# Optimization experiments

Measured on AMD Instinct MI355X. Metric: run time of the kernel, lower is better.

Reference implementation:

```python
import jax, jax.numpy as jnp
import numpy as np

C = 64          # channels
K = 7           # 19 - 6*num with num=2 (conv_first, avg_pool, snake kernel size)
GN_GROUPS = C // 4


def conv2d(x, w, b=None, pad=(0, 0), groups=1):
    out = jax.lax.conv_general_dilated(
        x, w, window_strides=(1, 1),
        padding=((pad[0], pad[0]), (pad[1], pad[1])),
        dimension_numbers=('NCHW', 'OIHW', 'NCHW'),
        feature_group_count=groups)
    if b is not None:
        out = out + b[None, :, None, None]
    return out


def avg_pool(x, k, pad):
    # torch AvgPool2d default count_include_pad=True -> always divide by k*k
    s = jax.lax.reduce_window(x, 0.0, jax.lax.add, (1, 1, k, k), (1, 1, 1, 1),
                              ((0, 0), (0, 0), (pad, pad), (pad, pad)))
    return s / float(k * k)


def bn_eval(x, g, b, m, v, eps):
    inv = g / jnp.sqrt(v + eps)
    return x * inv[None, :, None, None] + (b - m * inv)[None, :, None, None]


def group_norm(x, g, b, groups, eps=1e-5):
    B, Ch, H, W = x.shape
    xr = x.reshape(B, groups, Ch // groups, H, W)
    mu = xr.mean(axis=(2, 3, 4), keepdims=True)
    var = xr.var(axis=(2, 3, 4), keepdims=True)
    xr = (xr - mu) / jnp.sqrt(var + eps)
    return xr.reshape(B, Ch, H, W) * g[None, :, None, None] + b[None, :, None, None]


def cum_offset(off):
    # Faithful to DSCNet DSC: center point pinned to 0, offsets accumulate outward
    # via `for index in range(1, center)`. The two endpoints keep their RAW,
    # DETACHED offsets (original code's off-by-one quirk on the detached clone).
    k = off.shape[1]
    c = k // 2
    new = [None] * k
    new[c] = jnp.zeros_like(off[:, c])
    for i in range(1, c):
        new[c + i] = new[c + i - 1] + off[:, c + i]
        new[c - i] = new[c - i + 1] + off[:, c - i]
    new[0] = jax.lax.stop_gradient(off[:, 0])
    new[k - 1] = jax.lax.stop_gradient(off[:, k - 1])
    return jnp.stack(new, axis=1)


def bilinear(feat, y, x):
    # feat [B,C,R,Cc]; y,x [B,K,R,Cc] -> samples [B,C,K,R,Cc]
    B, Ch, R, Cc = feat.shape
    y0 = jnp.floor(y)
    x0 = jnp.floor(x)
    y0i = jnp.clip(y0.astype(jnp.int32), 0, R - 1)
    y1i = jnp.clip(y0.astype(jnp.int32) + 1, 0, R - 1)
    x0i = jnp.clip(x0.astype(jnp.int32), 0, Cc - 1)
    x1i = jnp.clip(x0.astype(jnp.int32) + 1, 0, Cc - 1)
    gather = jax.vmap(lambda f, yi, xi: f[:, yi, xi])  # [C,R,Cc],[K,R,Cc]->[C,K,R,Cc]
    va0 = gather(feat, y0i, x0i)
    vc0 = gather(feat, y0i, x1i)
    va1 = gather(feat, y1i, x0i)
    vc1 = gather(feat, y1i, x1i)
    # interpolation weights use coords clamped to [0, max+1] (faithful to original)
    y0f = jnp.clip(y0, 0.0, float(R))
    y1f = jnp.clip(y0 + 1.0, 0.0, float(R))
    x0f = jnp.clip(x0, 0.0, float(Cc))
    x1f = jnp.clip(x0 + 1.0, 0.0, float(Cc))
    wa0 = ((y1f - y) * (x1f - x))[:, None]
    wc0 = ((y1f - y) * (x - x0f))[:, None]
    wa1 = ((y - y0f) * (x1f - x))[:, None]
    wc1 = ((y - y0f) * (x - x0f))[:, None]
    return va0 * wa0 + vc0 * wc0 + va1 * wa1 + vc1 * wc1


def dsconv(x, off_w, off_b, bn_g, bn_b, bn_m, bn_v, dsc_w, dsc_b, gn_g, gn_b, morph):
    # Dynamic Snake Conv (extend_scope=1, if_offset=True)
    B, Ch, R, Cc = x.shape
    off = jnp.tanh(bn_eval(conv2d(x, off_w, off_b, (1, 1)), bn_g, bn_b, bn_m, bn_v, 1e-5))
    y_off, x_off = off[:, :K], off[:, K:]
    spread = (jnp.arange(K, dtype=x.dtype) - K // 2)[None, :, None, None]
    rows = jnp.arange(R, dtype=x.dtype)[None, None, :, None]
    cols = jnp.arange(Cc, dtype=x.dtype)[None, None, None, :]
    if morph == 0:  # kernel spreads along x, snake swings in y
        y = rows + cum_offset(y_off)
        xc = cols + spread
    else:           # kernel spreads along y, snake swings in x
        y = rows + spread
        xc = cols + cum_offset(x_off)
    y = jnp.broadcast_to(y, (B, K, R, Cc))
    xc = jnp.broadcast_to(xc, (B, K, R, Cc))
    samp = bilinear(x, y, xc)  # [B,C,K,R,Cc]
    # strided (K,1)/(1,K) conv over the deformed map == contraction over (in, k)
    out = jnp.einsum('oik,bikrc->borc', dsc_w, samp) + dsc_b[None, :, None, None]
    out = group_norm(out, gn_g, gn_b, GN_GROUPS)
    return jax.nn.relu(out)


def setup_inputs() -> dict:
    key = jax.random.key(0)
    kit = iter(jax.random.split(key, 64))

    def rn(shape):
        if len(shape) == 1:
            return jax.random.normal(next(kit), shape, jnp.float32) * 0.05
        fan_in = int(np.prod(shape[1:]))
        return jax.random.normal(next(kit), shape, jnp.float32) / np.sqrt(fan_in)

    B, H, W = 2, 192, 192
    d = {}
    d['x'] = jax.random.normal(next(kit), (B, C, H, W), jnp.float32)
    d['w_first'] = rn((C, C, K, K))
    d['hc1_w'] = rn((C, 1, 1, 9)); d['hc1_b'] = rn((C,))
    d['hc2_w'] = rn((C, 1, 1, 7)); d['hc2_b'] = rn((C,))
    d['hc3_w'] = rn((C, 1, 1, 5)); d['hc3_b'] = rn((C,))
    d['vc1_w'] = rn((C, 1, 9, 1)); d['vc1_b'] = rn((C,))
    d['vc2_w'] = rn((C, 1, 7, 1)); d['vc2_b'] = rn((C,))
    d['vc3_w'] = rn((C, 1, 5, 1)); d['vc3_b'] = rn((C,))
    for p in ('h', 'v'):
        d[p + '_off_w'] = rn((2 * K, C, 3, 3)); d[p + '_off_b'] = rn((2 * K,))
        d[p + '_bn_g'] = 1.0 + rn((2 * K,)); d[p + '_bn_b'] = rn((2 * K,))
        d[p + '_bn_m'] = rn((2 * K,))
        d[p + '_bn_v'] = jax.random.uniform(next(kit), (2 * K,), jnp.float32) + 0.5
        d[p + '_dsc_w'] = rn((C, C, K)); d[p + '_dsc_b'] = rn((C,))
        d[p + '_gn_g'] = 1.0 + rn((C,)); d[p + '_gn_b'] = rn((C,))
    d['last_w'] = rn((C, C, 1, 1))
    d['last_g'] = 1.0 + rn((C,)); d['last_b'] = rn((C,))
    d['last_m'] = rn((C,))
    d['last_v'] = jax.random.uniform(next(kit), (C,), jnp.float32) + 0.5
    return d


def reference(x, w_first, hc1_w, hc1_b, hc2_w, hc2_b, hc3_w, hc3_b,
              vc1_w, vc1_b, vc2_w, vc2_b, vc3_w, vc3_b,
              h_off_w, h_off_b, h_bn_g, h_bn_b, h_bn_m, h_bn_v,
              h_dsc_w, h_dsc_b, h_gn_g, h_gn_b,
              v_off_w, v_off_b, v_bn_g, v_bn_b, v_bn_m, v_bn_v,
              v_dsc_w, v_dsc_b, v_gn_g, v_gn_b,
              last_w, last_g, last_b, last_m, last_v):
    x1 = avg_pool(conv2d(x, w_first, None, (K // 2, K // 2)), K, K // 2)
    h = conv2d(x1, hc1_w, hc1_b, (0, 4), groups=C)
    h = conv2d(h, hc2_w, hc2_b, (0, 3), groups=C)
    h = conv2d(h, hc3_w, hc3_b, (0, 2), groups=C)
    h = dsconv(h, h_off_w, h_off_b, h_bn_g, h_bn_b, h_bn_m, h_bn_v,
               h_dsc_w, h_dsc_b, h_gn_g, h_gn_b, morph=0)
    v = conv2d(x1, vc1_w, vc1_b, (4, 0), groups=C)
    v = conv2d(v, vc2_w, vc2_b, (3, 0), groups=C)
    v = conv2d(v, vc3_w, vc3_b, (2, 0), groups=C)
    v = dsconv(v, v_off_w, v_off_b, v_bn_g, v_bn_b, v_bn_m, v_bn_v,
               v_dsc_w, v_dsc_b, v_gn_g, v_gn_b, morph=1)
    out = h + v + x1
    out = conv2d(out, last_w, None, (0, 0))          # 1x1, bias=False (norm present)
    out = bn_eval(out, last_g, last_b, last_m, last_v, 1e-3)
    return out * jax.nn.sigmoid(out)                  # SiLU
```

## Files before the change

### kernel.cpp

```cpp
#include <hip/hip_runtime.h>
#include <hip/hip_bf16.h>
#include <hip/hip_fp16.h>
#include <math.h>

#define Bq 2
#define Cq 64
#define Hq 192
#define Wq 192
#define HWq (Hq*Wq)
#define Nq ((size_t)Bq*Cq*HWq)

typedef __attribute__((ext_vector_type(8))) _Float16 f16x8;
typedef __attribute__((ext_vector_type(4))) float f32x4;

__device__ inline unsigned short h2us(__half h) {
  union { __half h; unsigned short u; } v; v.h = h; return v.u;
}

__global__ __launch_bounds__(256) void prep_all_kernel(
    const float* hc1_w, const float* hc1_b, const float* hc2_w, const float* hc2_b,
    const float* hc3_w, const float* hc3_b,
    const float* vc1_w, const float* vc1_b, const float* vc2_w, const float* vc2_b,
    const float* vc3_w, const float* vc3_b,
    const float* h_off_w, const float* h_off_b, const float* h_bn_g, const float* h_bn_b,
    const float* h_bn_m, const float* h_bn_v,
    const float* v_off_w, const float* v_off_b, const float* v_bn_g, const float* v_bn_b,
    const float* v_bn_m, const float* v_bn_v,
    const float* last_w, const float* last_g, const float* last_b, const float* last_m,
    const float* last_v,
    const float* __restrict__ w_first,
    const float* __restrict__ h_dsc_w, const float* __restrict__ v_dsc_w,
    float* wEffH, float* bEffH, float* wEffV, float* bEffV,
    float* wOffH, float* bOffH, float* wOffV, float* bOffV,
    float* lwT, float* lbO, float* wB,
    unsigned short* __restrict__ wtpH, unsigned short* __restrict__ wtpV,
    unsigned short* __restrict__ wpack)
{
  int bid = blockIdx.x;
  int t = threadIdx.x;
  if (bid == 0) {
    if (t < 128) {
      int ch = t & 63;
      bool ish = t < 64;
      const float* w1p = (ish ? hc1_w : vc1_w) + ch*9;
      const float* w2p = (ish ? hc2_w : vc2_w) + ch*7;
      const float* w3p = (ish ? hc3_w : vc3_w) + ch*5;
      float w1r[9], w2r[7], w3r[5];
#pragma unroll
      for (int j = 0; j < 9; j++) w1r[j] = w1p[j];
#pragma unroll
      for (int k = 0; k < 7; k++) w2r[k] = w2p[k];
#pragma unroll
      for (int m = 0; m < 5; m++) w3r[m] = w3p[m];
      float t15[15];
#pragma unroll
      for (int s = 0; s < 15; s++) {
        float a = 0.f;
#pragma unroll
        for (int j = 0; j < 9; j++) { int k2 = s - j; if (k2 >= 0 && k2 < 7) a += w1r[j]*w2r[k2]; }
        t15[s] = a;
      }
      float* we = (ish ? wEffH : wEffV) + ch*19;
#pragma unroll
      for (int s = 0; s < 19; s++) {
        float a = 0.f;
#pragma unroll
        for (int j = 0; j < 15; j++) { int k3 = s - j; if (k3 >= 0 && k3 < 5) a += t15[j]*w3r[k3]; }
        we[s] = a;
      }
      float S2 = 0.f, S3 = 0.f;
#pragma unroll
      for (int j = 0; j < 7; j++) S2 += w2r[j];
#pragma unroll
      for (int j = 0; j < 5; j++) S3 += w3r[j];
      float b1 = (ish ? hc1_b : vc1_b)[ch];
      float b2 = (ish ? hc2_b : vc2_b)[ch];
      float b3 = (ish ? hc3_b : vc3_b)[ch];
      (ish ? bEffH : bEffV)[ch] = b1*S2*S3 + b2*S3 + b3;
    }
    for (int idx = t; idx < 9*64*7; idx += 256) {
      int tap = idx / 448; int rem = idx % 448; int i = rem / 7; int m = rem % 7;
      float invh = h_bn_g[m] / sqrtf(h_bn_v[m] + 1e-5f);
      wOffH[(tap*64 + i)*8 + m] = h_off_w[(m*64 + i)*9 + tap] * invh;
      float invv = v_bn_g[7+m] / sqrtf(v_bn_v[7+m] + 1e-5f);
      wOffV[(tap*64 + i)*8 + m] = v_off_w[((7+m)*64 + i)*9 + tap] * invv;
    }
    if (t < 7) {
      float invh = h_bn_g[t] / sqrtf(h_bn_v[t] + 1e-5f);
      bOffH[t] = h_off_b[t]*invh + h_bn_b[t] - h_bn_m[t]*invh;
      float invv = v_bn_g[7+t] / sqrtf(v_bn_v[7+t] + 1e-5f);
      bOffV[t] = v_off_b[7+t]*invv + v_bn_b[7+t] - v_bn_m[7+t]*invv;
    }
    for (int idx = t; idx < 4096; idx += 256) {
      int o = idx % 64; int i = idx / 64;
      float inv = last_g[o] / sqrtf(last_v[o] + 1e-3f);
      lwT[i*64 + o] = last_w[o*64 + i] * inv;
    }
    if (t < 64) {
      float inv = last_g[t] / sqrtf(last_v[t] + 1e-3f);
      lbO[t] = last_b[t] - last_m[t]*inv;
    }
  } else if (bid <= 9) {
    int tid = (bid - 1)*256 + t;
    if (tid >= 2*64*18) return;
    int cls = tid % 18;
    int ch  = (tid / 18) % 64;
    int br  = tid / (18*64);
    int c = (cls < 9) ? cls : cls + 174;
    const float* w1p = (br==0 ? hc1_w : vc1_w) + ch*9;
    const float* w2p = (br==0 ? hc2_w : vc2_w) + ch*7;
    const float* w3p = (br==0 ? hc3_w : vc3_w) + ch*5;
    float b1 = (br==0 ? hc1_b : vc1_b)[ch];
    float b2 = (br==0 ? hc2_b : vc2_b)[ch];
    float b3 = (br==0 ? hc3_b : vc3_b)[ch];
    float w1r[9], w2r[7], w3r[5];
#pragma unroll
    for (int j = 0; j < 9; j++) w1r[j] = w1p[j];
#pragma unroll
    for (int k = 0; k < 7; k++) w2r[k] = w2p[k];
#pragma unroll
    for (int m = 0; m < 5; m++) w3r[m] = w3p[m];
    float acc[19];
#pragma unroll
    for (int s = 0; s < 19; s++) acc[s] = 0.f;
    float bacc = b3;
#pragma unroll
    for (int m = 0; m < 5; m++) {
      int d = c + m - 2;
      bool dok = (d >= 0 && d < Wq);
      float s2b = b2;
#pragma unroll
      for (int k = 0; k < 7; k++) {
        int e = d + k - 3;
        bool eok = (e >= 0 && e < Wq);
        if (eok) s2b += w2r[k] * b1;
        float wmk = w3r[m] * w2r[k];
#pragma unroll
        for (int j = 0; j < 9; j++) {
          int fd = e + j - 4;
          bool fok = (fd >= 0 && fd < Wq);
          float contrib = (dok && eok && fok) ? wmk * w1r[j] : 0.f;
          acc[m + k + j] += contrib;
        }
      }
      if (dok) bacc += w3r[m] * s2b;
    }
    float* dst = wB + ((size_t)(br*64 + ch)*18 + cls)*20;
#pragma unroll
    for (int s = 0; s < 19; s++) dst[s] = acc[s];
    dst[19] = bacc;
  } else {
    int tid = (bid - 10)*256 + t;
    int nthr = 64*256;
    for (int idx = tid; idx < 7*2*2*64*32; idx += nthr) {
      int ch32 = idx & 31;
      int oc   = (idx >> 5) & 63;
      int hl   = (idx >> 11) & 1;
      int kc   = (idx >> 12) & 1;
      int tap  = idx >> 13;
      int i = kc*32 + ch32;
      float vh = h_dsc_w[oc*448 + i*7 + tap];
      float vv = v_dsc_w[oc*448 + i*7 + tap];
      _Float16 hh = (_Float16)vh;
      _Float16 hv = (_Float16)vv;
      unsigned short uh, uv;
      if (!hl) { uh = *(unsigned short*)&hh; uv = *(unsigned short*)&hv; }
      else {
        _Float16 lh = (_Float16)(vh - (float)hh);
        _Float16 lv = (_Float16)(vv - (float)hv);
        uh = *(unsigned short*)&lh; uv = *(unsigned short*)&lv;
      }
      wtpH[idx] = uh; wtpV[idx] = uv;
    }
    for (int e = tid; e < 2*49*2*64*32; e += nthr) {
      int ch  = e & 31;
      int oc  = (e >> 5) & 63;
      int hl  = (e >> 11) & 1;
      int rest = e >> 12;
      int tap = rest % 49;
      int h   = rest / 49;
      float wv = w_first[((size_t)oc*64 + h*32 + ch)*49 + tap];
      __half hh = __float2half(wv);
      unsigned short us;
      if (!hl) us = h2us(hh);
      else { float rr = wv - __half2float(hh); us = h2us(__float2half(rr)); }
      wpack[e] = us;
    }
  }
}

__global__ __launch_bounds__(192) void tof16_pack_kernel(const float* __restrict__ x,
                                                         unsigned short* __restrict__ xpack)
{
  __shared__ unsigned int s[192*64];
  int r = blockIdx.x, b = blockIdx.y;
  int t = threadIdx.x;
  for (int ch = 0; ch < 64; ch++) {
    float v = x[((size_t)(b*64+ch)*Hq + r)*Wq + t];
    _Float16 hh = (_Float16)v;
    s[t*64 + (ch ^ (t & 31))] = (unsigned int)*(unsigned short*)&hh;
  }
  __syncthreads();
  unsigned short* dst = xpack + ((size_t)b*Hq + r)*Wq*64;
  for (int i = 0; i < 8; i++) {
    int gidx = i*192 + t;
    int c = gidx >> 3, g = gidx & 7;
    unsigned short tmp[8];
#pragma unroll
    for (int j = 0; j < 8; j++) {
      int ch = g*8 + j;
      tmp[j] = (unsigned short)s[c*64 + (ch ^ (c & 31))];
    }
    uint4 v;
    v.x = (unsigned int)tmp[0] | ((unsigned int)tmp[1] << 16);
    v.y = (unsigned int)tmp[2] | ((unsigned int)tmp[3] << 16);
    v.z = (unsigned int)tmp[4] | ((unsigned int)tmp[5] << 16);
    v.w = (unsigned int)tmp[6] | ((unsigned int)tmp[7] << 16);
    *(uint4*)(dst + (size_t)gidx*8) = v;
  }
}

__global__ __launch_bounds__(256) void conv7_mfma_kernel(
    const unsigned short* __restrict__ xpack,
    const unsigned short* __restrict__ wpack,
    float* __restrict__ out)
{
  __shared__ __align__(16) unsigned short sA[8*54*32];
  int ct = blockIdx.x;
  int rt = blockIdx.y;
  int b  = blockIdx.z;
  int r0 = rt*2, c0 = ct*48;
  int t = threadIdx.x;
  int wv = t >> 6;
  int l  = t & 63;
  int l15 = l & 15, lg = l >> 4;
  int oc = wv*16 + l15;

  f32x4 acc[2][3];
#pragma unroll
  for (int i = 0; i < 2; i++)
#pragma unroll
    for (int j = 0; j < 3; j++) acc[i][j] = (f32x4){0.f,0.f,0.f,0.f};

  for (int h = 0; h < 2; h++) {
    __syncthreads();
    for (int idx = t; idx < 8*54*4; idx += 256) {
      int g = idx & 3, pix = idx >> 2;
      int row = pix / 54, col = pix % 54;
      int gr = r0 - 3 + row, gc = c0 - 3 + col;
      uint4 v = {0u,0u,0u,0u};
      if (gr >= 0 && gr < Hq && gc >= 0 && gc < Wq)
        v = *(const uint4*)(xpack + (((size_t)b*Hq + gr)*Wq + gc)*64 + (h*4 + g)*8);
      ((uint4*)sA)[(row*54 + col)*4 + (g ^ ((col >> 1) & 3))] = v;
    }
    __syncthreads();
    const unsigned short* wb = wpack + (size_t)h*49*4096;
#pragma unroll 7
    for (int tap = 0; tap < 49; tap++) {
      int dy = tap / 7, dx = tap % 7;
      f16x8 bh = *(const f16x8*)(wb + (size_t)tap*4096 +        oc*32 + lg*8);
      f16x8 bl = *(const f16x8*)(wb + (size_t)tap*4096 + 2048 + oc*32 + lg*8);
#pragma unroll
      for (int rw = 0; rw < 2; rw++) {
        int arow = rw + dy;
        f16x8 a[3];
#pragma unroll
        for (int tc = 0; tc < 3; tc++) {
          int col = tc*16 + l15 + dx;
          a[tc] = *(const f16x8*)((const uint4*)sA + (arow*54 + col)*4 + (lg ^ ((col >> 1) & 3)));
        }
#pragma unroll
        for (int tc = 0; tc < 3; tc++) {
          acc[rw][tc] = __builtin_amdgcn_mfma_f32_16x16x32_f16(a[tc], bh, acc[rw][tc], 0, 0, 0);
          acc[rw][tc] = __builtin_amdgcn_mfma_f32_16x16x32_f16(a[tc], bl, acc[rw][tc], 0, 0, 0);
        }
      }
    }
  }
#pragma unroll
  for (int rw = 0; rw < 2; rw++) {
    float* dst = out + ((size_t)(b*64 + oc)*Hq + (r0 + rw))*Wq + c0;
#pragma unroll
    for (int tc = 0; tc < 3; tc++) {
      f32x4 v = acc[rw][tc];
      *(float4*)(dst + tc*16 + lg*4) = make_float4(v[0], v[1], v[2], v[3]);
    }
  }
}

__global__ __launch_bounds__(256) void pool_fused_kernel(const float* __restrict__ in,
                                                         float* __restrict__ out)
{
  __shared__ float raw[38][192];
  __shared__ float cs[32][192];
  int rt = blockIdx.x;
  int plane = blockIdx.y;
  int r0 = rt*32;
  int t = threadIdx.x;
  const float* src = in + (size_t)plane*HWq;
  for (int idx = t; idx < 38*192; idx += 256) {
    int lr = idx / 192, c = idx % 192;
    int gr = r0 - 3 + lr;
    raw[lr][c] = (gr >= 0 && gr < Hq) ? src[gr*Wq + c] : 0.f;
  }
  __syncthreads();
  for (int idx = t; idx < 32*192; idx += 256) {
    int lr = idx / 192, c = idx % 192;
    float s = 0.f;
#pragma unroll
    for (int dr = 0; dr < 7; dr++) s += raw[lr + dr][c];
    cs[lr][c] = s;
  }
  __syncthreads();
  float* dst = out + (size_t)plane*HWq + r0*Wq;
  for (int idx = t; idx < 32*192; idx += 256) {
    int lr = idx / 192, c = idx % 192;
    float s = 0.f;
#pragma unroll
    for (int dc = -3; dc <= 3; dc++) {
      int cc = c + dc;
      if (cc >= 0 && cc < Wq) s += cs[lr][cc];
    }
    dst[idx] = s * (1.f/49.f);
  }
}

__global__ __launch_bounds__(256) void dwf_kernel(const float* __restrict__ x1,
                                                  const float* __restrict__ wEffH,
                                                  const float* __restrict__ bEffH,
                                                  const float* __restrict__ wBH,
                                                  const float* __restrict__ wEffV,
                                                  const float* __restrict__ bEffV,
                                                  const float* __restrict__ wBV,
                                                  unsigned short* __restrict__ packH,
                                                  unsigned short* __restrict__ packV)
{
  __shared__ float sW[8][19][20];
  int z = blockIdx.z;
  int br = z >> 1, b = z & 1;
  const float* wEff = br ? wEffV : wEffH;
  const float* bEff = br ? bEffV : bEffH;
  const float* wB   = br ? wBV   : wBH;
  unsigned short* pack = br ? packV : packH;
  int g8 = blockIdx.y;
  int t = threadIdx.x;
  int chb = g8*8;
  for (int i = t; i < 8*380; i += 256) {
    int ch8 = i / 380; int rem = i % 380;
    int row = rem / 20, jj = rem % 20;
    int ch = chb + ch8;
    float v;
    if (row < 18) v = wB[((size_t)ch*18 + row)*20 + jj];
    else v = (jj < 19) ? wEff[ch*19 + jj] : bEff[ch];
    sW[ch8][row][jj] = v;
  }
  __syncthreads();
  int p = blockIdx.x*256 + t;
  int r = p / Wq, c = p % Wq;
  float vals[8];
  if (br == 0) {
    int row = (c < 9) ? c : ((c >= Wq-9) ? (c - 174) : 18);
#pragma unroll
    for (int ch8 = 0; ch8 < 8; ch8++) {
      const float* src = x1 + (size_t)(b*Cq + chb + ch8)*HWq + r*Wq;
      float s = sW[ch8][row][19];
#pragma unroll
      for (int j = 0; j < 19; j++) {
        int idx = min(max(c + j - 9, 0), Wq-1);
        s += src[idx] * sW[ch8][row][j];
      }
      vals[ch8] = s;
    }
  } else {
    int row = (r < 9) ? r : ((r >= Hq-9) ? (r - 174) : 18);
#pragma unroll
    for (int ch8 = 0; ch8 < 8; ch8++) {
      const float* src = x1 + (size_t)(b*Cq + chb + ch8)*HWq + c;
      float s = sW[ch8][row][19];
#pragma unroll
      for (int j = 0; j < 19; j++) {
        int idx = min(max(r + j - 9, 0), Hq-1);
        s += src[idx*Wq] * sW[ch8][row][j];
      }
      vals[ch8] = s;
    }
  }
  unsigned int hi[4], lo[4];
#pragma unroll
  for (int q = 0; q < 4; q++) {
    __half h0 = __float2half(vals[2*q]);
    __half h1 = __float2half(vals[2*q+1]);
    __half l0 = __float2half(vals[2*q]   - __half2float(h0));
    __half l1 = __float2half(vals[2*q+1] - __half2float(h1));
    hi[q] = (unsigned int)h2us(h0) | ((unsigned int)h2us(h1) << 16);
    lo[q] = (unsigned int)h2us(l0) | ((unsigned int)h2us(l1) << 16);
  }
  *(uint4*)(pack + (((size_t)b*16 + g8)*HWq + p)*8)     = make_uint4(hi[0], hi[1], hi[2], hi[3]);
  *(uint4*)(pack + (((size_t)b*16 + 8 + g8)*HWq + p)*8) = make_uint4(lo[0], lo[1], lo[2], lo[3]);
}

__global__ __launch_bounds__(256) void off_cum_kernel(const unsigned short* __restrict__ fpH,
                                                      const unsigned short* __restrict__ fpV,
                                                      const float* __restrict__ wOffH,
                                                      const float* __restrict__ bOffH,
                                                      const float* __restrict__ wOffV,
                                                      const float* __restrict__ bOffV,
                                                      float* __restrict__ hcum,
                                                      float* __restrict__ vcum)
{
  const size_t HW8 = (size_t)HWq*8;
  int bid = blockIdx.x;
  int xcd = bid & 7, lid = bid >> 3;
  int combo = xcd >> 1;
  int br = combo >> 1, b = combo & 1;
  int pxblk = (xcd & 1)*72 + lid;
  const unsigned short* fp = br ? fpV : fpH;
  const float* wOff = br ? wOffV : wOffH;
  const float* bOff = br ? bOffV : bOffH;
  float* cum = br ? vcum : hcum;
  int p = pxblk*256 + threadIdx.x;
  int r = p / Wq, c = p % Wq;
  float tv[7];
#pragma unroll
  for (int m = 0; m < 7; m++) tv[m] = bOff[m];
  const unsigned short* fb = fp + (size_t)b*HWq*128;
  for (int tap = 0; tap < 9; tap++) {
    int dy = tap/3 - 1, dx = tap%3 - 1;
    int rr = r + dy, cc = c + dx;
    if (rr < 0 || rr >= Hq || cc < 0 || cc >= Wq) continue;
    const unsigned short* p0 = fb + ((size_t)rr*Wq + cc)*8;
    const float* wp = wOff + tap*512;
    for (int g = 0; g < 8; g++) {
      f16x8 hv = *(const f16x8*)(p0 + (size_t)g*HW8);
      f16x8 lv = *(const f16x8*)(p0 + (size_t)(8 + g)*HW8);
#pragma unroll
      for (int e = 0; e < 8; e++) {
        float fv = (float)hv[e] + (float)lv[e];
        const float* wr = wp + (g*8 + e)*8;
#pragma unroll
        for (int m = 0; m < 7; m++) tv[m] += fv * wr[m];
      }
    }
  }
#pragma unroll
  for (int m = 0; m < 7; m++) tv[m] = tanhf(tv[m]);
  float c0 = tv[0], c1 = tv[1] + tv[2], c2 = tv[2], c3 = 0.f;
  float c4 = tv[4], c5 = tv[4] + tv[5], c6 = tv[6];
  size_t bb = (size_t)b*7*HWq + p;
  cum[bb + 0*HWq] = c0; cum[bb + 1*HWq] = c1; cum[bb + 2*HWq] = c2;
  cum[bb + 3*HWq] = c3; cum[bb + 4*HWq] = c4; cum[bb + 5*HWq] = c5;
  cum[bb + 6*HWq] = c6;
}

__global__ __launch_bounds__(128) void einsum_mfma_kernel(
    const unsigned short* __restrict__ fpH, const unsigned short* __restrict__ fpV,
    const float* __restrict__ cumH, const float* __restrict__ cumV,
    const unsigned short* __restrict__ wtpHp, const unsigned short* __restrict__ wtpVp,
    const float* __restrict__ dscbH, const float* __restrict__ dscbV,
    float* __restrict__ outH, float* __restrict__ outV,
    float* __restrict__ pstat)
{
  __shared__ __align__(16) unsigned short sA[2*128*64];
  const size_t HW8 = (size_t)HWq*8;
  int morph = blockIdx.y;
  const unsigned short* fp  = morph ? fpV   : fpH;
  const float* cum          = morph ? cumV  : cumH;
  const unsigned short* wtp = morph ? wtpVp : wtpHp;
  const float* dsc_b        = morph ? dscbV : dscbH;
  float* out                = morph ? outV  : outH;
  int bid = blockIdx.x;
  int swz = (bid & 7)*72 + (bid >> 3);
  int b   = swz / 288;
  int blk = swz % 288;
  int t = threadIdx.x;
  int w = t >> 6, l = t & 63;
  int l15 = l & 15, lg = l >> 4;
  int l7 = l15 & 7;
  int p = blk*128 + w*64 + l;
  int r = p / Wq, c = p % Wq;

  f32x4 acc[4][4];
#pragma unroll
  for (int i = 0; i < 4; i++)
#pragma unroll
    for (int j = 0; j < 4; j++) acc[i][j] = (f32x4){0.f,0.f,0.f,0.f};

  const unsigned short* fb = fp + (size_t)b*HWq*128;

  for (int kp = 0; kp < 4; kp++) {
    int k0 = kp*2;
    int nk = (kp < 3) ? 2 : 1;
    for (int kk = 0; kk < nk; kk++) {
      int k = k0 + kk;
      unsigned short* myrow = sA + (size_t)(kk*128 + w*64 + l)*64;
      bool oob;
      const unsigned short *p0, *p1;
      float w0, w1;
      if (morph == 0) {
        int xi = c + k - 3;
        oob = (xi < 0 || xi >= Wq);
        if (!oob) {
          float y = (float)r + cum[((size_t)(b*7 + k))*HWq + p];
          float y0 = floorf(y);
          int y0q = (int)y0;
          int y0i = min(max(y0q, 0), Hq-1);
          int y1i = min(max(y0q + 1, 0), Hq-1);
          float y0f = fminf(fmaxf(y0, 0.f), (float)Hq);
          float y1f = fminf(fmaxf(y0 + 1.f, 0.f), (float)Hq);
          w0 = y1f - y; w1 = y - y0f;
          p0 = fb + ((size_t)y0i*Wq + xi)*8;
          p1 = fb + ((size_t)y1i*Wq + xi)*8;
        }
      } else {
        int yi = r + k - 3;
        oob = (yi < 0 || yi >= Hq);
        if (!oob) {
          float xf = (float)c + cum[((size_t)(b*7 + k))*HWq + p];
          float x0 = floorf(xf);
          int x0q = (int)x0;
          int x0i = min(max(x0q, 0), Wq-1);
          int x1i = min(max(x0q + 1, 0), Wq-1);
          float x0f = fminf(fmaxf(x0, 0.f), (float)Wq);
          float x1f = fminf(fmaxf(x0 + 1.f, 0.f), (float)Wq);
          w0 = x1f - xf; w1 = xf - x0f;
          p0 = fb + ((size_t)yi*Wq + x0i)*8;
          p1 = fb + ((size_t)yi*Wq + x1i)*8;
        }
      }
      if (oob) {
        uint4 z = {0u,0u,0u,0u};
#pragma unroll
        for (int j = 0; j < 8; j++) ((uint4*)myrow)[j] = z;
      } else {
#pragma unroll
        for (int g = 0; g < 8; g++) {
          f16x8 a0h = *(const f16x8*)(p0 + (size_t)g*HW8);
          f16x8 a1h = *(const f16x8*)(p1 + (size_t)g*HW8);
          f16x8 sh;
#pragma unroll
          for (int e = 0; e < 8; e++) {
            float v = w0*(float)a0h[e] + w1*(float)a1h[e];
            sh[e] = (_Float16)v;
          }
          *(f16x8*)(myrow + (size_t)(g ^ l7)*8) = sh;
        }
      }
    }
    for (int kk = 0; kk < nk; kk++) {
      int k = k0 + kk;
#pragma unroll
      for (int kc = 0; kc < 2; kc++) {
        const unsigned short* wbase = wtp + (size_t)((k*2 + kc)*2)*2048;
        f16x8 bh[4], bl[4];
#pragma unroll
        for (int tb = 0; tb < 4; tb++) {
          bh[tb] = *(const f16x8*)(wbase + (tb*16 + l15)*32 + lg*8);
          bl[tb] = *(const f16x8*)(wbase + 2048 + (tb*16 + l15)*32 + lg*8);
        }
        f16x8 ah[4];
#pragma unroll
        for (int ta = 0; ta < 4; ta++) {
          const unsigned short* rbase = sA + (size_t)(kk*128 + w*64 + ta*16 + l15)*64;
          ah[ta] = *(const f16x8*)(rbase + (size_t)((kc*4 + lg) ^ l7)*8);
        }
#pragma unroll
        for (int ta = 0; ta < 4; ta++)
#pragma unroll
          for (int tb = 0; tb < 4; tb++) {
            acc[ta][tb] = __builtin_amdgcn_mfma_f32_16x16x32_f16(ah[ta], bh[tb], acc[ta][tb], 0, 0, 0);
            acc[ta][tb] = __builtin_amdgcn_mfma_f32_16x16x32_f16(ah[ta], bl[tb], acc[ta][tb], 0, 0, 0);
          }
      }
    }
  }
  int pbase = blk*128 + w*64;
#pragma unroll
  for (int tb = 0; tb < 4; tb++) {
    int oc = tb*16 + l15;
    float bias = dsc_b[oc];
    float* dst = out + (size_t)(b*64 + oc)*HWq + pbase;
    float s = 0.f, ss = 0.f;
#pragma unroll
    for (int ta = 0; ta < 4; ta++) {
      f32x4 v = acc[ta][tb];
      float v0 = v[0]+bias, v1 = v[1]+bias, v2 = v[2]+bias, v3 = v[3]+bias;
      *(float4*)(dst + ta*16 + lg*4) = make_float4(v0, v1, v2, v3);
      s  += v0 + v1 + v2 + v3;
      ss += v0*v0 + v1*v1 + v2*v2 + v3*v3;
    }
    s  += __shfl_xor(s, 16);
    s  += __shfl_xor(s, 32);
    ss += __shfl_xor(ss, 16);
    ss += __shfl_xor(ss, 32);
    if (lg == 0) {
      float* pp = pstat + ((size_t)(morph*576 + swz)*2 + w)*128 + oc*2;
      pp[0] = s; pp[1] = ss;
    }
  }
}

__global__ __launch_bounds__(256) void gnred_kernel(const float* __restrict__ pstat,
                                                    float* __restrict__ stats)
{
  int combo = blockIdx.x;
  int buf = combo >> 7;
  int rem = combo & 127;
  int b = rem >> 6, ch = rem & 63;
  int t = threadIdx.x;
  float s = 0.f, ss = 0.f;
  for (int q = t; q < 576; q += 256) {
    int blk = q >> 1, w = q & 1;
    const float* pp = pstat + ((size_t)(buf*576 + b*288 + blk)*2 + w)*128 + ch*2;
    s += pp[0]; ss += pp[1];
  }
  __shared__ float red[2][4];
  for (int off = 32; off; off >>= 1) {
    s  += __shfl_down(s, off);
    ss += __shfl_down(ss, off);
  }
  if ((t & 63) == 0) { red[0][t >> 6] = s; red[1][t >> 6] = ss; }
  __syncthreads();
  if (t == 0) {
    s  = red[0][0] + red[0][1] + red[0][2] + red[0][3];
    ss = red[1][0] + red[1][1] + red[1][2] + red[1][3];
    stats[combo*2 + 0] = s;
    stats[combo*2 + 1] = ss;
  }
}

__global__ __launch_bounds__(256) void gnfinal_kernel(const float* __restrict__ stats,
                                                      const float* __restrict__ h_gn_g, const float* __restrict__ h_gn_b,
                                                      const float* __restrict__ v_gn_g, const float* __restrict__ v_gn_b,
                                                      float* __restrict__ gnAB)
{
  int t = threadIdx.x;
  int buf = t >> 7, ch = t & 63;
  int base = t & ~3;
  float sum = 0.f, ss = 0.f;
#pragma unroll
  for (int q = 0; q < 4; q++) { sum += stats[(base+q)*2]; ss += stats[(base+q)*2 + 1]; }
  const float n = 4.f * HWq;
  float mean = sum / n;
  float var = ss / n - mean*mean;
  float gg = (buf ? v_gn_g : h_gn_g)[ch];
  float bb = (buf ? v_gn_b : h_gn_b)[ch];
  float A = gg / sqrtf(var + 1e-5f);
  gnAB[t*2 + 0] = A;
  gnAB[t*2 + 1] = bb - mean*A;
}

__global__ __launch_bounds__(256) void final2_kernel(const float* __restrict__ hbuf,
                                                     const float* __restrict__ vbuf,
                                                     const float* __restrict__ x1,
                                                     const float* __restrict__ gnAB,
                                                     const float* __restrict__ lwT,
                                                     const float* __restrict__ lbO,
                                                     float* __restrict__ out)
{
  int b = blockIdx.y;
  int p = blockIdx.x*256 + threadIdx.x;
  float acc[64];
#pragma unroll
  for (int o = 0; o < 64; o++) acc[o] = 0.f;
  for (int i = 0; i < 64; i++) {
    size_t off = (size_t)(b*64 + i)*HWq + p;
    int plane = b*64 + i;
    int ih = plane*2;
    int iv = (128 + plane)*2;
    float hv = fmaxf(hbuf[off]*gnAB[ih] + gnAB[ih+1], 0.f);
    float vv = fmaxf(vbuf[off]*gnAB[iv] + gnAB[iv+1], 0.f);
    float cv = hv + vv + x1[off];
    const float* wr = lwT + i*64;
#pragma unroll
    for (int o = 0; o < 64; o++) acc[o] += cv * wr[o];
  }
  float* dst = out + (size_t)b*Cq*HWq + p;
#pragma unroll
  for (int o = 0; o < 64; o++) {
    float yv = acc[o] + lbO[o];
    dst[(size_t)o*HWq] = yv / (1.f + expf(-yv));
  }
}

extern "C" void kernel_launch(void* const* d_in, const int* in_sizes, int n_in,
                              void* d_out, int out_size, void* d_ws, size_t ws_size,
                              hipStream_t stream)
{
  const float* x       = (const float*)d_in[0];
  const float* w_first = (const float*)d_in[1];
  float* ws = (float*)d_ws;

  float* bufA = ws;
  float* bufB = ws + Nq;
  float* x1   = ws + 2*Nq;
  float* h_ds = ws + 3*Nq;
  float* v_ds = ws + 4*Nq;
  size_t off = 5*Nq;
  float* hcum  = ws + off; off += (size_t)Bq*7*HWq;
  float* vcum  = ws + off; off += (size_t)Bq*7*HWq;
  float* wEffH = ws + off; off += 64*19;
  float* bEffH = ws + off; off += 64;
  float* wEffV = ws + off; off += 64*19;
  float* bEffV = ws + off; off += 64;
  float* wtH   = ws + off; off += 64*64*7;
  float* wtV   = ws + off; off += 64*64*7;
  float* wOffH = ws + off; off += 9*64*8;
  float* bOffH = ws + off; off += 8;
  float* wOffV = ws + off; off += 9*64*8;
  float* bOffV = ws + off; off += 8;
  float* lwT   = ws + off; off += 64*64;
  float* lbO   = ws + off; off += 64;
  float* stats = ws + off; off += 512;
  float* gnAB  = ws + off; off += 512;
  float* wB    = ws + off; off += 2*64*18*20;
  float* pstat = ws + off; off += (size_t)2*576*2*128;
  unsigned short* wpack = (unsigned short*)(ws + off); off += 2*49*2*64*32/2 + 16;
  unsigned short* xpack  = (unsigned short*)h_ds;
  unsigned short* fpackH = (unsigned short*)h_ds;
  unsigned short* fpackV = (unsigned short*)v_ds;
  unsigned short* wtpH = (unsigned short*)wtH;
  unsigned short* wtpV = (unsigned short*)wtV;

  prep_all_kernel<<<dim3(74), dim3(256), 0, stream>>>(
      (const float*)d_in[2],  (const float*)d_in[3],  (const float*)d_in[4],  (const float*)d_in[5],
      (const float*)d_in[6],  (const float*)d_in[7],
      (const float*)d_in[8],  (const float*)d_in[9],  (const float*)d_in[10], (const float*)d_in[11],
      (const float*)d_in[12], (const float*)d_in[13],
      (const float*)d_in[14], (const float*)d_in[15], (const float*)d_in[16], (const float*)d_in[17],
      (const float*)d_in[18], (const float*)d_in[19],
      (const float*)d_in[24], (const float*)d_in[25], (const float*)d_in[26], (const float*)d_in[27],
      (const float*)d_in[28], (const float*)d_in[29],
      (const float*)d_in[34], (const float*)d_in[35], (const float*)d_in[36], (const float*)d_in[37],
      (const float*)d_in[38],
      w_first, (const float*)d_in[20], (const float*)d_in[30],
      wEffH, bEffH, wEffV, bEffV, wOffH, bOffH, wOffV, bOffV, lwT, lbO, wB,
      wtpH, wtpV, wpack);

  tof16_pack_kernel<<<dim3(Hq, Bq), dim3(192), 0, stream>>>(x, xpack);
  conv7_mfma_kernel<<<dim3(4, 96, 2), dim3(256), 0, stream>>>(xpack, wpack, bufA);

  pool_fused_kernel<<<dim3(6, 128), dim3(256), 0, stream>>>(bufA, x1);

  dwf_kernel<<<dim3(144, 8, 4), dim3(256), 0, stream>>>(x1, wEffH, bEffH, wB,
      wEffV, bEffV, wB + 64*18*20, fpackH, fpackV);

  off_cum_kernel<<<dim3(576), dim3(256), 0, stream>>>(fpackH, fpackV,
      wOffH, bOffH, wOffV, bOffV, hcum, vcum);

  einsum_mfma_kernel<<<dim3(576, 2), dim3(128), 0, stream>>>(fpackH, fpackV,
      hcum, vcum, wtpH, wtpV, (const float*)d_in[21], (const float*)d_in[31], bufA, bufB, pstat);

  gnred_kernel<<<dim3(256), dim3(256), 0, stream>>>(pstat, stats);
  gnfinal_kernel<<<dim3(1), dim3(256), 0, stream>>>(stats,
      (const float*)d_in[22], (const float*)d_in[23],
      (const float*)d_in[32], (const float*)d_in[33], gnAB);

  final2_kernel<<<dim3(144, 2), dim3(256), 0, stream>>>(bufA, bufB, x1, gnAB, lwT, lbO, (float*)d_out);
}
```

Before: 302.1 us.

## Shrink einsum MFMA blocks to single wave of 32 pixels

Restructures the deformable-conv einsum kernel so each block is one 64-thread wave handling 32 pixels instead of two waves handling 128. The bilinear gather into LDS is split so two half-waves each fill four of the eight channel groups, and the accumulator tile shrinks from 4x4 to 2x4. The grid quadruples, and the GroupNorm partial-stat layout and reduction kernel are resized to match. The aim is more blocks, less LDS and fewer registers per block for better occupancy and latency hiding, at the cost of reloading the weight fragments for each smaller pixel tile.

Measured after the change: 306.8 us. No clear change (+1.6%).

```diff
diff --git a/kernel.cpp b/kernel.cpp
--- a/kernel.cpp
+++ b/kernel.cpp
@@ -452,7 +452,7 @@
   cum[bb + 6*HWq] = c6;
 }
 
-__global__ __launch_bounds__(128) void einsum_mfma_kernel(
+__global__ __launch_bounds__(64, 4) void einsum_mfma_kernel(
     const unsigned short* __restrict__ fpH, const unsigned short* __restrict__ fpV,
     const float* __restrict__ cumH, const float* __restrict__ cumV,
     const unsigned short* __restrict__ wtpHp, const unsigned short* __restrict__ wtpVp,
@@ -460,7 +460,7 @@
     float* __restrict__ outH, float* __restrict__ outV,
     float* __restrict__ pstat)
 {
-  __shared__ __align__(16) unsigned short sA[2*128*64];
+  __shared__ __align__(16) unsigned short sA[2*32*64];
   const size_t HW8 = (size_t)HWq*8;
   int morph = blockIdx.y;
   const unsigned short* fp  = morph ? fpV   : fpH;
@@ -469,19 +469,20 @@
   const float* dsc_b        = morph ? dscbV : dscbH;
   float* out                = morph ? outV  : outH;
   int bid = blockIdx.x;
-  int swz = (bid & 7)*72 + (bid >> 3);
-  int b   = swz / 288;
-  int blk = swz % 288;
-  int t = threadIdx.x;
-  int w = t >> 6, l = t & 63;
+  int swz = (bid & 7)*288 + (bid >> 3);
+  int b   = swz / 1152;
+  int blk = swz % 1152;
+  int l = threadIdx.x;
   int l15 = l & 15, lg = l >> 4;
-  int l7 = l15 & 7;
-  int p = blk*128 + w*64 + l;
+  int l7 = l & 7;
+  int px5 = l & 31;
+  int chh = l >> 5;
+  int p = blk*32 + px5;
   int r = p / Wq, c = p % Wq;
 
-  f32x4 acc[4][4];
-#pragma unroll
-  for (int i = 0; i < 4; i++)
+  f32x4 acc[2][4];
+#pragma unroll
+  for (int i = 0; i < 2; i++)
 #pragma unroll
     for (int j = 0; j < 4; j++) acc[i][j] = (f32x4){0.f,0.f,0.f,0.f};
 
@@ -492,7 +493,7 @@
     int nk = (kp < 3) ? 2 : 1;
     for (int kk = 0; kk < nk; kk++) {
       int k = k0 + kk;
-      unsigned short* myrow = sA + (size_t)(kk*128 + w*64 + l)*64;
+      unsigned short* myrow = sA + (size_t)(kk*32 + px5)*64;
       bool oob;
       const unsigned short *p0, *p1;
       float w0, w1;
@@ -530,10 +531,14 @@
       if (oob) {
         uint4 z = {0u,0u,0u,0u};
 #pragma unroll
-        for (int j = 0; j < 8; j++) ((uint4*)myrow)[j] = z;
+        for (int gi = 0; gi < 4; gi++) {
+          int g = chh*4 + gi;
+          *(uint4*)(myrow + (size_t)(g ^ l7)*8) = z;
+        }
       } else {
 #pragma unroll
-        for (int g = 0; g < 8; g++) {
+        for (int gi = 0; gi < 4; gi++) {
+          int g = chh*4 + gi;
           f16x8 a0h = *(const f16x8*)(p0 + (size_t)g*HW8);
           f16x8 a1h = *(const f16x8*)(p1 + (size_t)g*HW8);
           f16x8 sh;
@@ -557,14 +562,14 @@
           bh[tb] = *(const f16x8*)(wbase + (tb*16 + l15)*32 + lg*8);
           bl[tb] = *(const f16x8*)(wbase + 2048 + (tb*16 + l15)*32 + lg*8);
         }
-        f16x8 ah[4];
-#pragma unroll
-        for (int ta = 0; ta < 4; ta++) {
-          const unsigned short* rbase = sA + (size_t)(kk*128 + w*64 + ta*16 + l15)*64;
+        f16x8 ah[2];
+#pragma unroll
+        for (int ta = 0; ta < 2; ta++) {
+          const unsigned short* rbase = sA + (size_t)(kk*32 + ta*16 + l15)*64;
           ah[ta] = *(const f16x8*)(rbase + (size_t)((kc*4 + lg) ^ l7)*8);
         }
 #pragma unroll
-        for (int ta = 0; ta < 4; ta++)
+        for (int ta = 0; ta < 2; ta++)
 #pragma unroll
           for (int tb = 0; tb < 4; tb++) {
             acc[ta][tb] = __builtin_amdgcn_mfma_f32_16x16x32_f16(ah[ta], bh[tb], acc[ta][tb], 0, 0, 0);
@@ -573,7 +578,7 @@
       }
     }
   }
-  int pbase = blk*128 + w*64;
+  int pbase = blk*32;
 #pragma unroll
   for (int tb = 0; tb < 4; tb++) {
     int oc = tb*16 + l15;
@@ -581,7 +586,7 @@
     float* dst = out + (size_t)(b*64 + oc)*HWq + pbase;
     float s = 0.f, ss = 0.f;
 #pragma unroll
-    for (int ta = 0; ta < 4; ta++) {
+    for (int ta = 0; ta < 2; ta++) {
       f32x4 v = acc[ta][tb];
       float v0 = v[0]+bias, v1 = v[1]+bias, v2 = v[2]+bias, v3 = v[3]+bias;
       *(float4*)(dst + ta*16 + lg*4) = make_float4(v0, v1, v2, v3);
@@ -593,7 +598,7 @@
     ss += __shfl_xor(ss, 16);
     ss += __shfl_xor(ss, 32);
     if (lg == 0) {
-      float* pp = pstat + ((size_t)(morph*576 + swz)*2 + w)*128 + oc*2;
+      float* pp = pstat + ((size_t)(morph*2304 + swz))*128 + oc*2;
       pp[0] = s; pp[1] = ss;
     }
   }
@@ -608,9 +613,8 @@
   int b = rem >> 6, ch = rem & 63;
   int t = threadIdx.x;
   float s = 0.f, ss = 0.f;
-  for (int q = t; q < 576; q += 256) {
-    int blk = q >> 1, w = q & 1;
-    const float* pp = pstat + ((size_t)(buf*576 + b*288 + blk)*2 + w)*128 + ch*2;
+  for (int q = t; q < 1152; q += 256) {
+    const float* pp = pstat + ((size_t)(buf*2304 + b*1152 + q))*128 + ch*2;
     s += pp[0]; ss += pp[1];
   }
   __shared__ float red[2][4];
@@ -713,7 +717,7 @@
   float* stats = ws + off; off += 512;
   float* gnAB  = ws + off; off += 512;
   float* wB    = ws + off; off += 2*64*18*20;
-  float* pstat = ws + off; off += (size_t)2*576*2*128;
+  float* pstat = ws + off; off += (size_t)2*2304*128;
   unsigned short* wpack = (unsigned short*)(ws + off); off += 2*49*2*64*32/2 + 16;
   unsigned short* xpack  = (unsigned short*)h_ds;
   unsigned short* fpackH = (unsigned short*)h_ds;
@@ -747,7 +751,7 @@
   off_cum_kernel<<<dim3(576), dim3(256), 0, stream>>>(fpackH, fpackV,
       wOffH, bOffH, wOffV, bOffV, hcum, vcum);
 
-  einsum_mfma_kernel<<<dim3(576, 2), dim3(128), 0, stream>>>(fpackH, fpackV,
+  einsum_mfma_kernel<<<dim3(2304, 2), dim3(64), 0, stream>>>(fpackH, fpackV,
       hcum, vcum, wtpH, wtpV, (const float*)d_in[21], (const float*)d_in[31], bufA, bufB, pstat);
 
   gnred_kernel<<<dim3(256), dim3(256), 0, stream>>>(pstat, stats);
```
